# Optimization experiments

Measured on AMD Instinct MI355X. Metric: run time of the kernel, lower is better.

## Reference

```python
import jax, jax.numpy as jnp
import numpy as np

NUM_HEADS = 16
HIDDEN = 1024
HEAD_DIM = HIDDEN // NUM_HEADS
B, S, D = 2, 2048, 1024


def setup_inputs() -> dict:
    key = jax.random.key(0)
    ks = jax.random.split(key, 7)
    scale = 1.0 / np.sqrt(D)
    return {
        "query": jax.random.normal(ks[0], (B, S, D), dtype=jnp.float32),
        "key": jax.random.normal(ks[1], (B, S, D), dtype=jnp.float32),
        "value": jax.random.normal(ks[2], (B, S, D), dtype=jnp.float32),
        "Wk_w": jax.random.normal(ks[3], (HIDDEN, D), dtype=jnp.float32) * scale,
        "Wk_b": jax.random.normal(ks[4], (HIDDEN,), dtype=jnp.float32) * scale,
        "Wv_w": jax.random.normal(ks[5], (HIDDEN, D), dtype=jnp.float32) * scale,
        "Wv_b": jax.random.normal(ks[6], (HIDDEN,), dtype=jnp.float32) * scale,
    }


def reference(query, key, value, Wk_w, Wk_b, Wv_w, Wv_b):
    # NOTE: in the original torch module, self.W_v is assigned twice, so the
    # SAME Linear (Wv) projects both key and value; Wk projects query.
    b, s, _ = query.shape

    def split_heads(x):  # [b,s,hidden] -> [b,h,s,hd]
        return x.reshape(b, s, NUM_HEADS, HEAD_DIM).transpose(0, 2, 1, 3)

    q = split_heads(query @ Wk_w.T + Wk_b)
    k = split_heads(key @ Wv_w.T + Wv_b)
    v = split_heads(value @ Wv_w.T + Wv_b)

    scores = jnp.einsum("bhqd,bhkd->bhqk", q, k) / jnp.sqrt(
        jnp.asarray(HEAD_DIM, dtype=q.dtype))
    probs = jax.nn.softmax(scores, axis=-1)
    out = jnp.einsum("bhqk,bhkd->bhqd", probs, v)
    return out.transpose(0, 2, 1, 3).reshape(b, s, NUM_HEADS * HEAD_DIM)
```

## Files before the change

kernel.cpp:

```cpp
#include <hip/hip_runtime.h>
#include <stdint.h>

typedef unsigned short u16;
typedef uint32_t u32;
typedef __bf16 bf16x8 __attribute__((ext_vector_type(8)));
typedef float f32x4 __attribute__((ext_vector_type(4)));
typedef u16 u16x4 __attribute__((ext_vector_type(4)));
typedef u16 u16x8 __attribute__((ext_vector_type(8)));

#define XQ_OFF 0ul
#define XK_OFF 4194304ul
#define XV_OFF 8388608ul
#define WK_OFF 12582912ul
#define WV_OFF 13631488ul
#define Q_OFF  14680064ul
#define K_OFF  18874368ul
#define V_OFF  23068672ul

#define SCQ 0.18033688011112042f

#if __has_builtin(__builtin_amdgcn_exp2f)
#define EXP2F(x) __builtin_amdgcn_exp2f(x)
#else
#define EXP2F(x) exp2f(x)
#endif

__device__ __forceinline__ u16 f2bf(float f) {
  u32 u = __float_as_uint(f);
  u32 r = (u + 0x7fffu + ((u >> 16) & 1u)) >> 16;
  return (u16)r;
}

__device__ __forceinline__ u32 pk2(float a, float b) {
  typedef __bf16 bf2_t __attribute__((ext_vector_type(2)));
  typedef float f2_t __attribute__((ext_vector_type(2)));
  f2_t v; v[0] = a; v[1] = b;
  bf2_t h = __builtin_convertvector(v, bf2_t);
  union { bf2_t h; u32 u; } cv; cv.h = h; return cv.u;
}

__device__ __forceinline__ void load_lds16(const void* g, void* l) {
  __builtin_amdgcn_global_load_lds(
      (const __attribute__((address_space(1))) u32*)g,
      (__attribute__((address_space(3))) u32*)l, 16, 0, 0);
}

__global__ __launch_bounds__(256) void cvt_tile_kernel(
    const float* __restrict__ xq, const float* __restrict__ xk,
    const float* __restrict__ xv, const float* __restrict__ wk,
    const float* __restrict__ wv, u16* __restrict__ ws) {
  __shared__ u16 tile[4096];
  const int bid = blockIdx.x;
  const float* src; size_t dstbase; int rt, ktp;
  if (bid < 3072) {
    int m = bid >> 10, loc = bid & 1023;
    src = (m == 0) ? xq : (m == 1) ? xk : xv;
    dstbase = (size_t)m * 4194304ul;
    rt = loc >> 4; ktp = loc & 15;
  } else {
    int r2 = bid - 3072;
    int m = r2 >> 8, loc = r2 & 255;
    src = m ? wv : wk;
    dstbase = WK_OFF + (size_t)m * 1048576ul;
    rt = loc >> 4; ktp = loc & 15;
  }
  const int t = threadIdx.x;
  const int row0 = t >> 4, c = t & 15;
  const int k = c * 4;
  const float* s = src + (size_t)(rt * 64 + row0) * 1024ul + ktp * 64 + k;
#pragma unroll
  for (int i = 0; i < 4; ++i) {
    float4 v = *(const float4*)(s + (size_t)i * 16384ul);
    int row = row0 + i * 16;
    u32* p = (u32*)(tile + ((k >> 5) * 2048 + ((k >> 3) & 3) * 512 + row * 8 + (k & 7)));
    p[0] = pk2(v.x, v.y);
    p[1] = pk2(v.z, v.w);
  }
  __syncthreads();
  u16* dst = ws + dstbase + (size_t)(rt * 32 + ktp * 2) * 2048ul;
#pragma unroll
  for (int so = 0; so < 4096; so += 2048)
    *(u16x8*)(dst + so + t * 8) = *(const u16x8*)(tile + so + t * 8);
}

__global__ __launch_bounds__(256) void proj_kernel(u16* __restrict__ ws,
                                                   const float* __restrict__ bk,
                                                   const float* __restrict__ bv) {
  const int proj = blockIdx.z;
  const int mtile = blockIdx.x;
  const int ntile = blockIdx.y;
  const u16* A = ws + (size_t)proj * 4194304ul;
  const u16* Bw = ws + ((proj == 0) ? WK_OFF : WV_OFF);
  const float* bias = (proj == 0) ? bk : bv;
  u16* outQ = ws + Q_OFF;
  u16* outK = ws + K_OFF;
  u16* outV = ws + V_OFF;

  __shared__ u16 As[2][4096];
  __shared__ u16 Bs[2][4096];

  const int t = threadIdx.x;
  const int w = t >> 6, lane = t & 63, g = lane >> 4, c = lane & 15;
  const int wm = w >> 1, wn = w & 1;
  const int off = t * 16;

  const char* Ag = (const char*)(A + (size_t)(2 * mtile) * 65536ul);
  const char* Bg = (const char*)(Bw + (size_t)(2 * ntile) * 65536ul);

  f32x4 acc[4][4];
#pragma unroll
  for (int mt = 0; mt < 4; ++mt)
#pragma unroll
    for (int nt = 0; nt < 4; ++nt) acc[mt][nt] = (f32x4){0.f, 0.f, 0.f, 0.f};

  load_lds16(Ag + off, (char*)As[0] + off);
  load_lds16(Ag + 131072 + off, (char*)As[0] + 4096 + off);
  load_lds16(Bg + off, (char*)Bs[0] + off);
  load_lds16(Bg + 131072 + off, (char*)Bs[0] + 4096 + off);
  __syncthreads();

#pragma unroll 1
  for (int kk = 0; kk < 32; ++kk) {
    const int cur = kk & 1;
    if (kk < 31) {
      const char* An = Ag + (size_t)(kk + 1) * 4096ul;
      const char* Bn = Bg + (size_t)(kk + 1) * 4096ul;
      char* Ad = (char*)As[cur ^ 1];
      char* Bd = (char*)Bs[cur ^ 1];
      load_lds16(An + off, Ad + off);
      load_lds16(An + 131072 + off, Ad + 4096 + off);
      load_lds16(Bn + off, Bd + off);
      load_lds16(Bn + 131072 + off, Bd + 4096 + off);
    }
    const u16* Ac = As[cur];
    const u16* Bc = Bs[cur];
    bf16x8 af[4], bf[4];
#pragma unroll
    for (int mt = 0; mt < 4; ++mt)
      af[mt] = *(const bf16x8*)(Ac + wm * 2048 + g * 512 + (mt * 16 + c) * 8);
#pragma unroll
    for (int nt = 0; nt < 4; ++nt)
      bf[nt] = *(const bf16x8*)(Bc + wn * 2048 + g * 512 + (nt * 16 + c) * 8);
#pragma unroll
    for (int mt = 0; mt < 4; ++mt)
#pragma unroll
      for (int nt = 0; nt < 4; ++nt)
        acc[mt][nt] = __builtin_amdgcn_mfma_f32_16x16x32_bf16(af[mt], bf[nt], acc[mt][nt], 0, 0, 0);
    __syncthreads();
  }

  const int m0 = mtile * 128 + wm * 64, n0 = ntile * 128 + wn * 64;
#pragma unroll
  for (int nt = 0; nt < 4; ++nt) {
    const int col = n0 + nt * 16 + c;
    const float bvv = bias[col];
    const int h = col >> 6, d = col & 63;
#pragma unroll
    for (int mt = 0; mt < 4; ++mt) {
      const int mbase = m0 + mt * 16 + g * 4;
      const int b = mbase >> 11;
      const int bh = b * 16 + h;
      if (proj == 2) {
        const int s = mbase & 2047;
        u16x4 pk;
#pragma unroll
        for (int r = 0; r < 4; ++r) pk[r] = f2bf(acc[mt][nt][r] + bvv);
        size_t idx = (size_t)bh * 131072ul + (size_t)(s >> 6) * 4096ul +
                     (size_t)((s & 63) >> 3) * 512ul + (size_t)d * 8ul + (size_t)(s & 7);
        *(u16x4*)(outV + idx) = pk;
      } else {
        u16* dst = (proj == 0) ? outQ : outK;
#pragma unroll
        for (int r = 0; r < 4; ++r) {
          const int m = mbase + r;
          const int s = m & 2047;
          float y = acc[mt][nt][r] + bvv;
          if (proj == 0) y *= SCQ;
          size_t idx;
          if (proj == 0)
            idx = (size_t)bh * 131072ul + (size_t)(s >> 7) * 8192ul + (size_t)(d >> 3) * 1024ul +
                  (size_t)(s & 127) * 8ul + (size_t)(d & 7);
          else
            idx = (size_t)bh * 131072ul + (size_t)(s >> 6) * 4096ul + (size_t)(d >> 3) * 512ul +
                  (size_t)(s & 63) * 8ul + (size_t)(d & 7);
          dst[idx] = f2bf(y);
        }
      }
    }
  }
}

__global__ __launch_bounds__(256, 2) void attn_kernel(const u16* __restrict__ ws,
                                                      float* __restrict__ out) {
  const int bh = blockIdx.x, qtile = blockIdx.y;
  const int b = bh >> 4, h = bh & 15;
  const int t = threadIdx.x, w = t >> 6, lane = t & 63, g = lane >> 4, c = lane & 15;

  __shared__ u16 Ks[2][4096];
  __shared__ u16 Vs[2][4096];
  __shared__ __align__(16) u16 Ps[4][1280];

  const u16* Qg = ws + Q_OFF + (size_t)bh * 131072ul + (size_t)qtile * 8192ul;
  const u16* Kg = ws + K_OFF + (size_t)bh * 131072ul;
  const u16* Vg = ws + V_OFF + (size_t)bh * 131072ul;

  const int off = t * 16;
  load_lds16((const char*)Kg + off, (char*)Ks[0] + off);
  load_lds16((const char*)Kg + 4096 + off, (char*)Ks[0] + 4096 + off);
  load_lds16((const char*)Vg + off, (char*)Vs[0] + off);
  load_lds16((const char*)Vg + 4096 + off, (char*)Vs[0] + 4096 + off);

  bf16x8 qf[2][2];
#pragma unroll
  for (int ntq = 0; ntq < 2; ++ntq)
#pragma unroll
    for (int ks = 0; ks < 2; ++ks)
      qf[ntq][ks] = *(const bf16x8*)(Qg + (ks * 4 + g) * 1024 + (w * 32 + ntq * 16 + c) * 8);

  u16x8 ou;
#pragma unroll
  for (int i = 0; i < 8; ++i) ou[i] = (u16)0x3F80;
  union { u16x8 u; bf16x8 b; } ocv; ocv.u = ou;
  const bf16x8 onesf = ocv.b;

  f32x4 O[2][4], Lacc[2];
#pragma unroll
  for (int mtq = 0; mtq < 2; ++mtq) {
    Lacc[mtq] = (f32x4){0.f, 0.f, 0.f, 0.f};
#pragma unroll
    for (int nt = 0; nt < 4; ++nt) O[mtq][nt] = (f32x4){0.f, 0.f, 0.f, 0.f};
  }

  u16* Psw = Ps[w];
  __syncthreads();

#pragma unroll 1
  for (int j = 0; j < 32; ++j) {
    const int cur = j & 1;
    if (j < 31) {
      const char* Kn = (const char*)(Kg + (size_t)(j + 1) * 4096ul);
      const char* Vn = (const char*)(Vg + (size_t)(j + 1) * 4096ul);
      char* Kd = (char*)Ks[cur ^ 1];
      char* Vd = (char*)Vs[cur ^ 1];
      load_lds16(Kn + off, Kd + off);
      load_lds16(Kn + 4096 + off, Kd + 4096 + off);
      load_lds16(Vn + off, Vd + off);
      load_lds16(Vn + 4096 + off, Vd + 4096 + off);
    }
    const u16* Kc = Ks[cur];
    const u16* Vc = Vs[cur];

    f32x4 St[4][2];
#pragma unroll
    for (int mtk = 0; mtk < 4; ++mtk)
#pragma unroll
      for (int ntq = 0; ntq < 2; ++ntq) St[mtk][ntq] = (f32x4){0.f, 0.f, 0.f, 0.f};
#pragma unroll
    for (int ks = 0; ks < 2; ++ks) {
      bf16x8 kf[4];
#pragma unroll
      for (int mtk = 0; mtk < 4; ++mtk)
        kf[mtk] = *(const bf16x8*)(Kc + (ks * 4 + g) * 512 + (mtk * 16 + c) * 8);
#pragma unroll
      for (int mtk = 0; mtk < 4; ++mtk)
#pragma unroll
        for (int ntq = 0; ntq < 2; ++ntq)
          St[mtk][ntq] =
              __builtin_amdgcn_mfma_f32_16x16x32_bf16(kf[mtk], qf[ntq][ks], St[mtk][ntq], 0, 0, 0);
    }
#pragma unroll
    for (int mtk = 0; mtk < 4; ++mtk)
#pragma unroll
      for (int ntq = 0; ntq < 2; ++ntq)
#pragma unroll
        for (int r = 0; r < 4; ++r) St[mtk][ntq][r] = EXP2F(St[mtk][ntq][r]);
#pragma unroll
    for (int ksh = 0; ksh < 2; ++ksh) {
#pragma unroll
      for (int ntq = 0; ntq < 2; ++ntq)
#pragma unroll
        for (int m2 = 0; m2 < 2; ++m2) {
          const int mtk = ksh * 2 + m2;
          u32 lo = pk2(St[mtk][ntq][0], St[mtk][ntq][1]);
          u32 hi = pk2(St[mtk][ntq][2], St[mtk][ntq][3]);
          u32* p = (u32*)(Psw + (ntq * 16 + c) * 40 + m2 * 16 + g * 4);
          p[0] = lo; p[1] = hi;
        }
      asm volatile("s_waitcnt lgkmcnt(0)" ::: "memory");
      bf16x8 pf[2], vf[4];
#pragma unroll
      for (int mtq = 0; mtq < 2; ++mtq)
        pf[mtq] = *(const bf16x8*)(Psw + (mtq * 16 + c) * 40 + g * 8);
#pragma unroll
      for (int nt = 0; nt < 4; ++nt)
        vf[nt] = *(const bf16x8*)(Vc + (ksh * 4 + g) * 512 + (nt * 16 + c) * 8);
#pragma unroll
      for (int mtq = 0; mtq < 2; ++mtq) {
        Lacc[mtq] = __builtin_amdgcn_mfma_f32_16x16x32_bf16(pf[mtq], onesf, Lacc[mtq], 0, 0, 0);
#pragma unroll
        for (int nt = 0; nt < 4; ++nt)
          O[mtq][nt] = __builtin_amdgcn_mfma_f32_16x16x32_bf16(pf[mtq], vf[nt], O[mtq][nt], 0, 0, 0);
      }
    }
    __syncthreads();
  }

  const int q0 = qtile * 128 + w * 32;
#pragma unroll
  for (int mtq = 0; mtq < 2; ++mtq)
#pragma unroll
    for (int r = 0; r < 4; ++r) {
      const float inv = 1.0f / Lacc[mtq][r];
      const int q = q0 + mtq * 16 + g * 4 + r;
      float* rowp = out + (size_t)(b * 2048 + q) * 1024ul + h * 64;
#pragma unroll
      for (int nt = 0; nt < 4; ++nt) rowp[nt * 16 + c] = O[mtq][nt][r] * inv;
    }
}

extern "C" void kernel_launch(void* const* d_in, const int* in_sizes, int n_in,
                              void* d_out, int out_size, void* d_ws, size_t ws_size,
                              hipStream_t stream) {
  const float* q = (const float*)d_in[0];
  const float* k = (const float*)d_in[1];
  const float* v = (const float*)d_in[2];
  const float* wk = (const float*)d_in[3];
  const float* bk = (const float*)d_in[4];
  const float* wv = (const float*)d_in[5];
  const float* bv = (const float*)d_in[6];
  u16* ws = (u16*)d_ws;
  float* out = (float*)d_out;

  cvt_tile_kernel<<<3584, 256, 0, stream>>>(q, k, v, wk, wv, ws);
  proj_kernel<<<dim3(32, 8, 3), 256, 0, stream>>>(ws, bk, bv);
  attn_kernel<<<dim3(32, 16), 256, 0, stream>>>(ws, out);
}
```

Measured before the change: 196.3 us.

## Load projection GEMM fragments directly from global memory into registers

The projection GEMM stops staging A and B tiles through double-buffered LDS with barriers. Each wave now reads its MFMA fragments straight from the pre-laid-out global workspace into registers, and a two-stage register ping-pong overlaps the next loads with the current MFMAs. This removes LDS traffic and the per-iteration __syncthreads. In exchange, the waves sharing a row or column of tiles now each read the same data from global memory, which doubles global/L2 traffic, and register pressure rises.

```diff
diff --git a/kernel.cpp b/kernel.cpp
--- a/kernel.cpp
+++ b/kernel.cpp
@@ -96,16 +96,12 @@
   u16* outK = ws + K_OFF;
   u16* outV = ws + V_OFF;
 
-  __shared__ u16 As[2][4096];
-  __shared__ u16 Bs[2][4096];
-
   const int t = threadIdx.x;
   const int w = t >> 6, lane = t & 63, g = lane >> 4, c = lane & 15;
   const int wm = w >> 1, wn = w & 1;
-  const int off = t * 16;
-
-  const char* Ag = (const char*)(A + (size_t)(2 * mtile) * 65536ul);
-  const char* Bg = (const char*)(Bw + (size_t)(2 * ntile) * 65536ul);
+
+  const u16* Aw = A + (size_t)(2 * mtile + wm) * 65536ul + (size_t)g * 512ul + (size_t)c * 8ul;
+  const u16* Bb = Bw + (size_t)(2 * ntile + wn) * 65536ul + (size_t)g * 512ul + (size_t)c * 8ul;
 
   f32x4 acc[4][4];
 #pragma unroll
@@ -113,40 +109,41 @@
 #pragma unroll
     for (int nt = 0; nt < 4; ++nt) acc[mt][nt] = (f32x4){0.f, 0.f, 0.f, 0.f};
 
-  load_lds16(Ag + off, (char*)As[0] + off);
-  load_lds16(Ag + 131072 + off, (char*)As[0] + 4096 + off);
-  load_lds16(Bg + off, (char*)Bs[0] + off);
-  load_lds16(Bg + 131072 + off, (char*)Bs[0] + 4096 + off);
-  __syncthreads();
+  bf16x8 a0[4], b0[4], a1[4], b1[4];
+#pragma unroll
+  for (int mt = 0; mt < 4; ++mt) {
+    a0[mt] = *(const bf16x8*)(Aw + (size_t)(mt * 16) * 8ul);
+    b0[mt] = *(const bf16x8*)(Bb + (size_t)(mt * 16) * 8ul);
+  }
 
 #pragma unroll 1
-  for (int kk = 0; kk < 32; ++kk) {
-    const int cur = kk & 1;
-    if (kk < 31) {
-      const char* An = Ag + (size_t)(kk + 1) * 4096ul;
-      const char* Bn = Bg + (size_t)(kk + 1) * 4096ul;
-      char* Ad = (char*)As[cur ^ 1];
-      char* Bd = (char*)Bs[cur ^ 1];
-      load_lds16(An + off, Ad + off);
-      load_lds16(An + 131072 + off, Ad + 4096 + off);
-      load_lds16(Bn + off, Bd + off);
-      load_lds16(Bn + 131072 + off, Bd + 4096 + off);
-    }
-    const u16* Ac = As[cur];
-    const u16* Bc = Bs[cur];
-    bf16x8 af[4], bf[4];
+  for (int kk = 0; kk < 32; kk += 2) {
+    const u16* An1 = Aw + (size_t)(kk + 1) * 2048ul;
+    const u16* Bn1 = Bb + (size_t)(kk + 1) * 2048ul;
+#pragma unroll
+    for (int mt = 0; mt < 4; ++mt) {
+      a1[mt] = *(const bf16x8*)(An1 + (size_t)(mt * 16) * 8ul);
+      b1[mt] = *(const bf16x8*)(Bn1 + (size_t)(mt * 16) * 8ul);
+    }
 #pragma unroll
     for (int mt = 0; mt < 4; ++mt)
-      af[mt] = *(const bf16x8*)(Ac + wm * 2048 + g * 512 + (mt * 16 + c) * 8);
-#pragma unroll
-    for (int nt = 0; nt < 4; ++nt)
-      bf[nt] = *(const bf16x8*)(Bc + wn * 2048 + g * 512 + (nt * 16 + c) * 8);
+#pragma unroll
+      for (int nt = 0; nt < 4; ++nt)
+        acc[mt][nt] = __builtin_amdgcn_mfma_f32_16x16x32_bf16(a0[mt], b0[nt], acc[mt][nt], 0, 0, 0);
+    if (kk + 2 < 32) {
+      const u16* An2 = Aw + (size_t)(kk + 2) * 2048ul;
+      const u16* Bn2 = Bb + (size_t)(kk + 2) * 2048ul;
+#pragma unroll
+      for (int mt = 0; mt < 4; ++mt) {
+        a0[mt] = *(const bf16x8*)(An2 + (size_t)(mt * 16) * 8ul);
+        b0[mt] = *(const bf16x8*)(Bn2 + (size_t)(mt * 16) * 8ul);
+      }
+    }
 #pragma unroll
     for (int mt = 0; mt < 4; ++mt)
 #pragma unroll
       for (int nt = 0; nt < 4; ++nt)
-        acc[mt][nt] = __builtin_amdgcn_mfma_f32_16x16x32_bf16(af[mt], bf[nt], acc[mt][nt], 0, 0, 0);
-    __syncthreads();
+        acc[mt][nt] = __builtin_amdgcn_mfma_f32_16x16x32_bf16(a1[mt], b1[nt], acc[mt][nt], 0, 0, 0);
   }
 
   const int m0 = mtile * 128 + wm * 64, n0 = ntile * 128 + wn * 64;
```

New measurement: 192.8 us. No clear change (-1.8%).
